# Kernel optimization log

Hardware: AMD Instinct MI355X
Metric: run time of the kernel (lower is better)

## Reference

```python
import jax, jax.numpy as jnp
import numpy as np

BS = 128  # block size for weight scale blocks

def dequant_block(w, s):
    # w: [O, I] fp8-valued weights (stored fp32 here); s: [O/BS, I/BS] per-block scale_inv
    O, I = w.shape
    sf = jnp.repeat(jnp.repeat(s, BS, axis=0), BS, axis=1)[:O, :I]
    return w * sf

def setup_inputs() -> dict:
    key = jax.random.key(0)
    ks = jax.random.split(key, 7)
    T, H, F = 512, 7168, 2048
    x = jax.random.normal(ks[0], (T, H), dtype=jnp.float32)
    w_gate = jax.random.normal(ks[1], (F, H), dtype=jnp.float32)
    s_gate = jax.random.uniform(ks[2], (F // BS, H // BS), dtype=jnp.float32, minval=0.01, maxval=0.05)
    w_up = jax.random.normal(ks[3], (F, H), dtype=jnp.float32)
    s_up = jax.random.uniform(ks[4], (F // BS, H // BS), dtype=jnp.float32, minval=0.01, maxval=0.05)
    w_down = jax.random.normal(ks[5], (H, F), dtype=jnp.float32)
    s_down = jax.random.uniform(ks[6], (H // BS, F // BS), dtype=jnp.float32, minval=0.01, maxval=0.05)
    return {"x": x, "w_gate": w_gate, "s_gate": s_gate, "w_up": w_up, "s_up": s_up,
            "w_down": w_down, "s_down": s_down}

def reference(x, w_gate, s_gate, w_up, s_up, w_down, s_down):
    # SwiGLU MLP with block-dequantized FP8 weights: down(silu(gate(x)) * up(x))
    wg = dequant_block(w_gate, s_gate)   # [F, H]
    wu = dequant_block(w_up, s_up)       # [F, H]
    wd = dequant_block(w_down, s_down)   # [H, F]
    g = x @ wg.T                          # [T, F]
    u = x @ wu.T                          # [T, F]
    h = jax.nn.silu(g) * u                # [T, F]
    return h @ wd.T                       # [T, H]
```

## Files before the change

### kernel.cpp

```cpp
#include <hip/hip_runtime.h>
#include <hip/hip_bf16.h>

typedef __bf16 bf16x8_t __attribute__((ext_vector_type(8)));
typedef float f32x4_t __attribute__((ext_vector_type(4)));

#define MFMA_BF16(a, b, c) __builtin_amdgcn_mfma_f32_16x16x32_bf16((a), (b), (c), 0, 0, 0)
#define VMW(N) asm volatile("s_waitcnt vmcnt(" #N ")" ::: "memory")
#define BARRIER() __builtin_amdgcn_s_barrier()

static constexpr int T_DIM = 512;
static constexpr int H_DIM = 7168;
static constexpr int F_DIM = 2048;

__device__ __forceinline__ ushort f2bf(float f) {
    return __builtin_bit_cast(ushort, __float2bfloat16(f));
}

__device__ __forceinline__ void gload_lds16(const void* g, void* l) {
    __builtin_amdgcn_global_load_lds(
        (const __attribute__((address_space(1))) unsigned int*)g,
        (__attribute__((address_space(3))) unsigned int*)(uintptr_t)l,
        16, 0, 0);
}

__global__ void cvt_x_kernel(const float* __restrict__ in, ushort* __restrict__ outp, int n4) {
    int i = blockIdx.x * 256 + threadIdx.x;
    if (i < n4) {
        float4 v = reinterpret_cast<const float4*>(in)[i];
        ushort4 o;
        o.x = f2bf(v.x); o.y = f2bf(v.y); o.z = f2bf(v.z); o.w = f2bf(v.w);
        reinterpret_cast<ushort4*>(outp)[i] = o;
    }
}

__global__ __launch_bounds__(512, 2) void gate_up_kernel(
    const ushort* __restrict__ xb, const float* __restrict__ wg,
    const float* __restrict__ sg, const float* __restrict__ wu,
    const float* __restrict__ su, float* __restrict__ gp, int NTS)
{
    __shared__ ushort As[2][256 * 64];
    __shared__ float  Bs[2][128 * 64];

    const int tid = threadIdx.x;
    const int lane = tid & 63;
    const int wid = tid >> 6;
    const int wr = wid >> 1, wc = wid & 1;
    const int bn = blockIdx.x, bm = blockIdx.y, bz = blockIdx.z;
    const int m0 = bm * 256;
    const int ks0 = bz * NTS, ks1 = ks0 + NTS;

    const float* __restrict__ Wb = (bn < 16) ? wg : wu;
    const float* __restrict__ srow = ((bn < 16) ? sg : su) + (size_t)(bn & 15) * (H_DIM / 128);
    const int nb = (bn & 15) * 128;

    f32x4_t acc[4][4] = {};

    const int a_r = tid >> 3, a_cu = tid & 7;
    const int b_r = tid >> 4, b_c32 = (tid & 15) >> 1, b_half = tid & 1;

    auto STAGE = [&](int kt, int bb) {
        const int k0 = kt * 64;
        #pragma unroll
        for (int q = 0; q < 4; ++q) {
            const int row = q * 64 + a_r;
            gload_lds16(&xb[(size_t)(m0 + row) * H_DIM + k0 + ((a_cu ^ (row & 7)) << 3)],
                        &As[bb][(q * 8192 + tid * 16) >> 1]);
        }
        #pragma unroll
        for (int q = 0; q < 4; ++q) {
            const int row = q * 32 + b_r;
            gload_lds16(&Wb[(size_t)(nb + row) * H_DIM + k0 + ((b_c32 ^ (row & 7)) << 3) + (b_half << 2)],
                        &Bs[bb][(q * 8192 + tid * 16) >> 2]);
        }
    };

    auto COMPUTE = [&](int bb) {
        #pragma unroll
        for (int ks = 0; ks < 2; ++ks) {
            const int kk = ks * 4 + (lane >> 4);
            bf16x8_t af[4];
            #pragma unroll
            for (int i = 0; i < 4; ++i) {
                const int row = wr * 64 + i * 16 + (lane & 15);
                af[i] = *reinterpret_cast<const bf16x8_t*>(&As[bb][row * 64 + ((kk ^ (row & 7)) << 3)]);
            }
            #pragma unroll
            for (int j = 0; j < 4; ++j) {
                const int row = wc * 64 + j * 16 + (lane & 15);
                const int u = kk ^ (row & 7);
                f32x4_t b0 = *reinterpret_cast<const f32x4_t*>(&Bs[bb][row * 64 + u * 8]);
                f32x4_t b1 = *reinterpret_cast<const f32x4_t*>(&Bs[bb][row * 64 + u * 8 + 4]);
                bf16x8_t bf;
                #pragma unroll
                for (int e = 0; e < 4; ++e) {
                    bf[e]     = (__bf16)b0[e];
                    bf[e + 4] = (__bf16)b1[e];
                }
                #pragma unroll
                for (int i = 0; i < 4; ++i)
                    acc[i][j] = MFMA_BF16(af[i], bf, acc[i][j]);
            }
        }
    };

    float s_cur = srow[ks0 >> 1];

    STAGE(ks0, 0);
    STAGE(ks0 + 1, 1);
    int bb = 0;
    for (int kt = ks0; kt < ks1; ++kt) {
        if (kt + 1 < ks1) { VMW(8); }
        else              { VMW(0); }
        BARRIER();
        if (((kt & 1) == 0) && kt > ks0) {
            const float s_new = srow[kt >> 1];
            const float r = s_cur / s_new;
            #pragma unroll
            for (int i = 0; i < 4; ++i)
                #pragma unroll
                for (int j = 0; j < 4; ++j)
                    acc[i][j] *= r;
            s_cur = s_new;
        }
        COMPUTE(bb);
        if (kt + 2 < ks1) {
            BARRIER();
            STAGE(kt + 2, bb);
        }
        bb ^= 1;
    }

    #pragma unroll
    for (int i = 0; i < 4; ++i)
        #pragma unroll
        for (int j = 0; j < 4; ++j)
            #pragma unroll
            for (int r = 0; r < 4; ++r) {
                const int m = m0 + wr * 64 + i * 16 + (lane >> 4) * 4 + r;
                const int nc = bn * 128 + wc * 64 + j * 16 + (lane & 15);
                gp[(size_t)bz * T_DIM * 4096 + (size_t)m * 4096 + nc] = acc[i][j][r] * s_cur;
            }
}

__global__ void h_reduce_kernel(const float* __restrict__ gp, ushort* __restrict__ hb,
                                int nsplit, int n4) {
    int i = blockIdx.x * 256 + threadIdx.x;
    if (i >= n4) return;
    const int m = i >> 9;
    const int c4 = i & 511;
    const size_t base = (size_t)m * 4096 + c4 * 4;
    const size_t stride = (size_t)T_DIM * 4096;
    float4 g = *reinterpret_cast<const float4*>(&gp[base]);
    float4 u = *reinterpret_cast<const float4*>(&gp[base + 2048]);
    for (int s = 1; s < nsplit; ++s) {
        float4 g2 = *reinterpret_cast<const float4*>(&gp[s * stride + base]);
        float4 u2 = *reinterpret_cast<const float4*>(&gp[s * stride + base + 2048]);
        g.x += g2.x; g.y += g2.y; g.z += g2.z; g.w += g2.w;
        u.x += u2.x; u.y += u2.y; u.z += u2.z; u.w += u2.w;
    }
    ushort4 o;
    o.x = f2bf(g.x / (1.0f + __expf(-g.x)) * u.x);
    o.y = f2bf(g.y / (1.0f + __expf(-g.y)) * u.y);
    o.z = f2bf(g.z / (1.0f + __expf(-g.z)) * u.z);
    o.w = f2bf(g.w / (1.0f + __expf(-g.w)) * u.w);
    reinterpret_cast<ushort4*>(hb)[i] = o;
}

template <bool DIRECT>
__global__ __launch_bounds__(512, 2) void down_kernel(
    const ushort* __restrict__ hb, const float* __restrict__ wd,
    const float* __restrict__ sd, float* __restrict__ outp, int NTS)
{
    __shared__ ushort As[2][128 * 64];
    __shared__ float  Bs[2][128 * 64];

    const int tid = threadIdx.x;
    const int lane = tid & 63;
    const int wid = tid >> 6;
    const int wr = wid >> 1, wc = wid & 1;
    const int bn = blockIdx.x, bm = blockIdx.y, bz = blockIdx.z;
    const int m0 = bm * 128;
    const float* __restrict__ srow = sd + (size_t)bn * (F_DIM / 128);
    const int nb = bn * 128;
    const int ks0 = bz * NTS, ks1 = ks0 + NTS;

    f32x4_t acc[2][4] = {};

    const int a_r = tid >> 3, a_cu = tid & 7;
    const int b_r = tid >> 4, b_c32 = (tid & 15) >> 1, b_half = tid & 1;

    auto STAGE = [&](int kt, int bb) {
        const int k0 = kt * 64;
        #pragma unroll
        for (int q = 0; q < 2; ++q) {
            const int row = q * 64 + a_r;
            gload_lds16(&hb[(size_t)(m0 + row) * F_DIM + k0 + ((a_cu ^ (row & 7)) << 3)],
                        &As[bb][(q * 8192 + tid * 16) >> 1]);
        }
        #pragma unroll
        for (int q = 0; q < 4; ++q) {
            const int row = q * 32 + b_r;
            gload_lds16(&wd[(size_t)(nb + row) * F_DIM + k0 + ((b_c32 ^ (row & 7)) << 3) + (b_half << 2)],
                        &Bs[bb][(q * 8192 + tid * 16) >> 2]);
        }
    };

    auto COMPUTE = [&](int bb) {
        #pragma unroll
        for (int ks = 0; ks < 2; ++ks) {
            const int kk = ks * 4 + (lane >> 4);
            bf16x8_t af[2];
            #pragma unroll
            for (int i = 0; i < 2; ++i) {
                const int row = wr * 32 + i * 16 + (lane & 15);
                af[i] = *reinterpret_cast<const bf16x8_t*>(&As[bb][row * 64 + ((kk ^ (row & 7)) << 3)]);
            }
            #pragma unroll
            for (int j = 0; j < 4; ++j) {
                const int row = wc * 64 + j * 16 + (lane & 15);
                const int u = kk ^ (row & 7);
                f32x4_t b0 = *reinterpret_cast<const f32x4_t*>(&Bs[bb][row * 64 + u * 8]);
                f32x4_t b1 = *reinterpret_cast<const f32x4_t*>(&Bs[bb][row * 64 + u * 8 + 4]);
                bf16x8_t bf;
                #pragma unroll
                for (int e = 0; e < 4; ++e) {
                    bf[e]     = (__bf16)b0[e];
                    bf[e + 4] = (__bf16)b1[e];
                }
                #pragma unroll
                for (int i = 0; i < 2; ++i)
                    acc[i][j] = MFMA_BF16(af[i], bf, acc[i][j]);
            }
        }
    };

    float s_cur = srow[ks0 >> 1];

    STAGE(ks0, 0);
    STAGE(ks0 + 1, 1);
    int bb = 0;
    for (int kt = ks0; kt < ks1; ++kt) {
        if (kt + 1 < ks1) { VMW(6); }
        else              { VMW(0); }
        BARRIER();
        if (((kt & 1) == 0) && kt > ks0) {
            const float s_new = srow[kt >> 1];
            const float r = s_cur / s_new;
            #pragma unroll
            for (int i = 0; i < 2; ++i)
                #pragma unroll
                for (int j = 0; j < 4; ++j)
                    acc[i][j] *= r;
            s_cur = s_new;
        }
        COMPUTE(bb);
        if (kt + 2 < ks1) {
            BARRIER();
            STAGE(kt + 2, bb);
        }
        bb ^= 1;
    }

    #pragma unroll
    for (int i = 0; i < 2; ++i)
        #pragma unroll
        for (int j = 0; j < 4; ++j)
            #pragma unroll
            for (int r = 0; r < 4; ++r) {
                const int m = m0 + wr * 32 + i * 16 + (lane >> 4) * 4 + r;
                const int nc = nb + wc * 64 + j * 16 + (lane & 15);
                const float v = acc[i][j][r] * s_cur;
                if (DIRECT)
                    outp[(size_t)m * H_DIM + nc] = v;
                else
                    outp[(size_t)bz * T_DIM * H_DIM + (size_t)m * H_DIM + nc] = v;
            }
}

__global__ void d_reduce_kernel(const float* __restrict__ dp, float* __restrict__ out, int n4) {
    int i = blockIdx.x * 256 + threadIdx.x;
    if (i >= n4) return;
    const size_t stride4 = (size_t)T_DIM * H_DIM / 4;
    float4 a = reinterpret_cast<const float4*>(dp)[i];
    float4 b = reinterpret_cast<const float4*>(dp)[i + stride4];
    a.x += b.x; a.y += b.y; a.z += b.z; a.w += b.w;
    reinterpret_cast<float4*>(out)[i] = a;
}

extern "C" void kernel_launch(void* const* d_in, const int* in_sizes, int n_in,
                              void* d_out, int out_size, void* d_ws, size_t ws_size,
                              hipStream_t stream) {
    const float* x  = (const float*)d_in[0];
    const float* wg = (const float*)d_in[1];
    const float* sg = (const float*)d_in[2];
    const float* wu = (const float*)d_in[3];
    const float* su = (const float*)d_in[4];
    const float* wd = (const float*)d_in[5];
    const float* sd = (const float*)d_in[6];
    float* out = (float*)d_out;

    ushort* xb = (ushort*)d_ws;
    ushort* hb = xb + (size_t)T_DIM * H_DIM;
    float*  gp = (float*)(hb + (size_t)T_DIM * F_DIM);

    const size_t base_b = (size_t)T_DIM * H_DIM * 2 + (size_t)T_DIM * F_DIM * 2;
    const size_t split_b = (size_t)T_DIM * 4096 * 4;

    int nsplit = 1;
    if (ws_size >= base_b + 4 * split_b) nsplit = 4;
    else if (ws_size >= base_b + 2 * split_b) nsplit = 2;

    const int n4x = T_DIM * H_DIM / 4;
    cvt_x_kernel<<<n4x / 256, 256, 0, stream>>>(x, xb, n4x);

    gate_up_kernel<<<dim3(32, T_DIM / 256, nsplit), 512, 0, stream>>>(
        xb, wg, sg, wu, su, gp, (H_DIM / 64) / nsplit);

    const int n4h = T_DIM * F_DIM / 4;
    h_reduce_kernel<<<n4h / 256, 256, 0, stream>>>(gp, hb, nsplit, n4h);

    const bool dsplit = (size_t)nsplit * split_b >= (size_t)2 * T_DIM * H_DIM * 4;
    if (dsplit) {
        float* dp = gp;
        down_kernel<false><<<dim3(H_DIM / 128, T_DIM / 128, 2), 512, 0, stream>>>(
            hb, wd, sd, dp, (F_DIM / 64) / 2);
        const int n4d = T_DIM * H_DIM / 4;
        d_reduce_kernel<<<n4d / 256, 256, 0, stream>>>(dp, out, n4d);
    } else {
        down_kernel<true><<<dim3(H_DIM / 128, T_DIM / 128, 1), 512, 0, stream>>>(
            hb, wd, sd, out, F_DIM / 64);
    }
}
```

Measured before the change: 110.1 us.

## Enlarge gate/up and down GEMM tiles to cut fp32 weight reloads

```diff
diff --git a/kernel.cpp b/kernel.cpp
--- a/kernel.cpp
+++ b/kernel.cpp
@@ -38,36 +38,40 @@
     const float* __restrict__ sg, const float* __restrict__ wu,
     const float* __restrict__ su, float* __restrict__ gp, int NTS)
 {
-    __shared__ ushort As[2][256 * 64];
-    __shared__ float  Bs[2][128 * 64];
+    __shared__ ushort As[256 * 64];
+    __shared__ float  Bs[2][256 * 64];
 
     const int tid = threadIdx.x;
     const int lane = tid & 63;
     const int wid = tid >> 6;
-    const int wr = wid >> 1, wc = wid & 1;
+    const int wr = wid >> 2, wcn = wid & 3;
     const int bn = blockIdx.x, bm = blockIdx.y, bz = blockIdx.z;
     const int m0 = bm * 256;
     const int ks0 = bz * NTS, ks1 = ks0 + NTS;
 
-    const float* __restrict__ Wb = (bn < 16) ? wg : wu;
-    const float* __restrict__ srow = ((bn < 16) ? sg : su) + (size_t)(bn & 15) * (H_DIM / 128);
-    const int nb = (bn & 15) * 128;
-
-    f32x4_t acc[4][4] = {};
+    const float* __restrict__ Wb = (bn < 8) ? wg : wu;
+    const float* __restrict__ srow = ((bn < 8) ? sg : su)
+        + (size_t)((bn & 7) * 2 + (wcn >> 1)) * (H_DIM / 128);
+    const int nb = (bn & 7) * 256;
+
+    f32x4_t acc[8][4] = {};
 
     const int a_r = tid >> 3, a_cu = tid & 7;
     const int b_r = tid >> 4, b_c32 = (tid & 15) >> 1, b_half = tid & 1;
 
-    auto STAGE = [&](int kt, int bb) {
+    auto STAGE_A = [&](int kt) {
         const int k0 = kt * 64;
         #pragma unroll
         for (int q = 0; q < 4; ++q) {
             const int row = q * 64 + a_r;
             gload_lds16(&xb[(size_t)(m0 + row) * H_DIM + k0 + ((a_cu ^ (row & 7)) << 3)],
-                        &As[bb][(q * 8192 + tid * 16) >> 1]);
-        }
-        #pragma unroll
-        for (int q = 0; q < 4; ++q) {
+                        &As[(q * 8192 + tid * 16) >> 1]);
+        }
+    };
+    auto STAGE_B = [&](int kt, int bb) {
+        const int k0 = kt * 64;
+        #pragma unroll
+        for (int q = 0; q < 8; ++q) {
             const int row = q * 32 + b_r;
             gload_lds16(&Wb[(size_t)(nb + row) * H_DIM + k0 + ((b_c32 ^ (row & 7)) << 3) + (b_half << 2)],
                         &Bs[bb][(q * 8192 + tid * 16) >> 2]);
@@ -78,15 +82,15 @@
         #pragma unroll
         for (int ks = 0; ks < 2; ++ks) {
             const int kk = ks * 4 + (lane >> 4);
-            bf16x8_t af[4];
-            #pragma unroll
-            for (int i = 0; i < 4; ++i) {
-                const int row = wr * 64 + i * 16 + (lane & 15);
-                af[i] = *reinterpret_cast<const bf16x8_t*>(&As[bb][row * 64 + ((kk ^ (row & 7)) << 3)]);
+            bf16x8_t af[8];
+            #pragma unroll
+            for (int i = 0; i < 8; ++i) {
+                const int row = wr * 128 + i * 16 + (lane & 15);
+                af[i] = *reinterpret_cast<const bf16x8_t*>(&As[row * 64 + ((kk ^ (row & 7)) << 3)]);
             }
             #pragma unroll
             for (int j = 0; j < 4; ++j) {
-                const int row = wc * 64 + j * 16 + (lane & 15);
+                const int row = wcn * 64 + j * 16 + (lane & 15);
                 const int u = kk ^ (row & 7);
                 f32x4_t b0 = *reinterpret_cast<const f32x4_t*>(&Bs[bb][row * 64 + u * 8]);
                 f32x4_t b1 = *reinterpret_cast<const f32x4_t*>(&Bs[bb][row * 64 + u * 8 + 4]);
@@ -97,7 +101,7 @@
                     bf[e + 4] = (__bf16)b1[e];
                 }
                 #pragma unroll
-                for (int i = 0; i < 4; ++i)
+                for (int i = 0; i < 8; ++i)
                     acc[i][j] = MFMA_BF16(af[i], bf, acc[i][j]);
             }
         }
@@ -105,39 +109,47 @@
 
     float s_cur = srow[ks0 >> 1];
 
-    STAGE(ks0, 0);
-    STAGE(ks0 + 1, 1);
+    STAGE_A(ks0);
+    STAGE_B(ks0, 0);
+    STAGE_B(ks0 + 1, 1);
+    VMW(8);
+    BARRIER();
+
     int bb = 0;
     for (int kt = ks0; kt < ks1; ++kt) {
-        if (kt + 1 < ks1) { VMW(8); }
-        else              { VMW(0); }
-        BARRIER();
         if (((kt & 1) == 0) && kt > ks0) {
             const float s_new = srow[kt >> 1];
             const float r = s_cur / s_new;
             #pragma unroll
-            for (int i = 0; i < 4; ++i)
+            for (int i = 0; i < 8; ++i)
                 #pragma unroll
                 for (int j = 0; j < 4; ++j)
                     acc[i][j] *= r;
             s_cur = s_new;
         }
         COMPUTE(bb);
-        if (kt + 2 < ks1) {
+        BARRIER();
+        if (kt + 1 < ks1) {
+            STAGE_A(kt + 1);
+            if (kt + 2 < ks1) {
+                STAGE_B(kt + 2, bb);
+                VMW(8);
+            } else {
+                VMW(0);
+            }
             BARRIER();
-            STAGE(kt + 2, bb);
         }
         bb ^= 1;
     }
 
     #pragma unroll
-    for (int i = 0; i < 4; ++i)
+    for (int i = 0; i < 8; ++i)
         #pragma unroll
         for (int j = 0; j < 4; ++j)
             #pragma unroll
             for (int r = 0; r < 4; ++r) {
-                const int m = m0 + wr * 64 + i * 16 + (lane >> 4) * 4 + r;
-                const int nc = bn * 128 + wc * 64 + j * 16 + (lane & 15);
+                const int m = m0 + wr * 128 + i * 16 + (lane >> 4) * 4 + r;
+                const int nc = bn * 256 + wcn * 64 + j * 16 + (lane & 15);
                 gp[(size_t)bz * T_DIM * 4096 + (size_t)m * 4096 + nc] = acc[i][j][r] * s_cur;
             }
 }
@@ -171,7 +183,7 @@
     const ushort* __restrict__ hb, const float* __restrict__ wd,
     const float* __restrict__ sd, float* __restrict__ outp, int NTS)
 {
-    __shared__ ushort As[2][128 * 64];
+    __shared__ ushort As[2][256 * 64];
     __shared__ float  Bs[2][128 * 64];
 
     const int tid = threadIdx.x;
@@ -179,12 +191,12 @@
     const int wid = tid >> 6;
     const int wr = wid >> 1, wc = wid & 1;
     const int bn = blockIdx.x, bm = blockIdx.y, bz = blockIdx.z;
-    const int m0 = bm * 128;
+    const int m0 = bm * 256;
     const float* __restrict__ srow = sd + (size_t)bn * (F_DIM / 128);
     const int nb = bn * 128;
     const int ks0 = bz * NTS, ks1 = ks0 + NTS;
 
-    f32x4_t acc[2][4] = {};
+    f32x4_t acc[4][4] = {};
 
     const int a_r = tid >> 3, a_cu = tid & 7;
     const int b_r = tid >> 4, b_c32 = (tid & 15) >> 1, b_half = tid & 1;
@@ -192,7 +204,7 @@
     auto STAGE = [&](int kt, int bb) {
         const int k0 = kt * 64;
         #pragma unroll
-        for (int q = 0; q < 2; ++q) {
+        for (int q = 0; q < 4; ++q) {
             const int row = q * 64 + a_r;
             gload_lds16(&hb[(size_t)(m0 + row) * F_DIM + k0 + ((a_cu ^ (row & 7)) << 3)],
                         &As[bb][(q * 8192 + tid * 16) >> 1]);
@@ -209,10 +221,10 @@
         #pragma unroll
         for (int ks = 0; ks < 2; ++ks) {
             const int kk = ks * 4 + (lane >> 4);
-            bf16x8_t af[2];
-            #pragma unroll
-            for (int i = 0; i < 2; ++i) {
-                const int row = wr * 32 + i * 16 + (lane & 15);
+            bf16x8_t af[4];
+            #pragma unroll
+            for (int i = 0; i < 4; ++i) {
+                const int row = wr * 64 + i * 16 + (lane & 15);
                 af[i] = *reinterpret_cast<const bf16x8_t*>(&As[bb][row * 64 + ((kk ^ (row & 7)) << 3)]);
             }
             #pragma unroll
@@ -228,7 +240,7 @@
                     bf[e + 4] = (__bf16)b1[e];
                 }
                 #pragma unroll
-                for (int i = 0; i < 2; ++i)
+                for (int i = 0; i < 4; ++i)
                     acc[i][j] = MFMA_BF16(af[i], bf, acc[i][j]);
             }
         }
@@ -240,14 +252,14 @@
     STAGE(ks0 + 1, 1);
     int bb = 0;
     for (int kt = ks0; kt < ks1; ++kt) {
-        if (kt + 1 < ks1) { VMW(6); }
+        if (kt + 1 < ks1) { VMW(8); }
         else              { VMW(0); }
         BARRIER();
         if (((kt & 1) == 0) && kt > ks0) {
             const float s_new = srow[kt >> 1];
             const float r = s_cur / s_new;
             #pragma unroll
-            for (int i = 0; i < 2; ++i)
+            for (int i = 0; i < 4; ++i)
                 #pragma unroll
                 for (int j = 0; j < 4; ++j)
                     acc[i][j] *= r;
@@ -262,12 +274,12 @@
     }
 
     #pragma unroll
-    for (int i = 0; i < 2; ++i)
+    for (int i = 0; i < 4; ++i)
         #pragma unroll
         for (int j = 0; j < 4; ++j)
             #pragma unroll
             for (int r = 0; r < 4; ++r) {
-                const int m = m0 + wr * 32 + i * 16 + (lane >> 4) * 4 + r;
+                const int m = m0 + wr * 64 + i * 16 + (lane >> 4) * 4 + r;
                 const int nc = nb + wc * 64 + j * 16 + (lane & 15);
                 const float v = acc[i][j][r] * s_cur;
                 if (DIRECT)
@@ -313,7 +325,7 @@
     const int n4x = T_DIM * H_DIM / 4;
     cvt_x_kernel<<<n4x / 256, 256, 0, stream>>>(x, xb, n4x);
 
-    gate_up_kernel<<<dim3(32, T_DIM / 256, nsplit), 512, 0, stream>>>(
+    gate_up_kernel<<<dim3(16, T_DIM / 256, nsplit), 512, 0, stream>>>(
         xb, wg, sg, wu, su, gp, (H_DIM / 64) / nsplit);
 
     const int n4h = T_DIM * F_DIM / 4;
@@ -322,12 +334,12 @@
     const bool dsplit = (size_t)nsplit * split_b >= (size_t)2 * T_DIM * H_DIM * 4;
     if (dsplit) {
         float* dp = gp;
-        down_kernel<false><<<dim3(H_DIM / 128, T_DIM / 128, 2), 512, 0, stream>>>(
+        down_kernel<false><<<dim3(H_DIM / 128, T_DIM / 256, 2), 512, 0, stream>>>(
             hb, wd, sd, dp, (F_DIM / 64) / 2);
         const int n4d = T_DIM * H_DIM / 4;
         d_reduce_kernel<<<n4d / 256, 256, 0, stream>>>(dp, out, n4d);
     } else {
-        down_kernel<true><<<dim3(H_DIM / 128, T_DIM / 128, 1), 512, 0, stream>>>(
+        down_kernel<true><<<dim3(H_DIM / 128, T_DIM / 256, 1), 512, 0, stream>>>(
             hb, wd, sd, out, F_DIM / 64);
     }
 }
```

Result: slower. 133.5 us (+21.3%).

## Stage fp32 weights through registers, convert to bf16 once into LDS

Applied to the files above, without the earlier changes.

```diff
diff --git a/kernel.cpp b/kernel.cpp
--- a/kernel.cpp
+++ b/kernel.cpp
@@ -6,6 +6,7 @@
 
 #define MFMA_BF16(a, b, c) __builtin_amdgcn_mfma_f32_16x16x32_bf16((a), (b), (c), 0, 0, 0)
 #define VMW(N) asm volatile("s_waitcnt vmcnt(" #N ")" ::: "memory")
+#define LGKM0() asm volatile("s_waitcnt lgkmcnt(0)" ::: "memory")
 #define BARRIER() __builtin_amdgcn_s_barrier()
 
 static constexpr int T_DIM = 512;
@@ -33,20 +34,20 @@
     }
 }
 
-__global__ __launch_bounds__(512, 2) void gate_up_kernel(
+__global__ __launch_bounds__(256, 2) void gate_up_kernel(
     const ushort* __restrict__ xb, const float* __restrict__ wg,
     const float* __restrict__ sg, const float* __restrict__ wu,
     const float* __restrict__ su, float* __restrict__ gp, int NTS)
 {
-    __shared__ ushort As[2][256 * 64];
-    __shared__ float  Bs[2][128 * 64];
+    __shared__ ushort As[2][128 * 64];
+    __shared__ ushort Bs[2][128 * 64];
 
     const int tid = threadIdx.x;
     const int lane = tid & 63;
     const int wid = tid >> 6;
     const int wr = wid >> 1, wc = wid & 1;
     const int bn = blockIdx.x, bm = blockIdx.y, bz = blockIdx.z;
-    const int m0 = bm * 256;
+    const int m0 = bm * 128;
     const int ks0 = bz * NTS, ks1 = ks0 + NTS;
 
     const float* __restrict__ Wb = (bn < 16) ? wg : wu;
@@ -56,21 +57,34 @@
     f32x4_t acc[4][4] = {};
 
     const int a_r = tid >> 3, a_cu = tid & 7;
-    const int b_r = tid >> 4, b_c32 = (tid & 15) >> 1, b_half = tid & 1;
-
-    auto STAGE = [&](int kt, int bb) {
+    const int b_row = tid >> 1, b_half = tid & 1;
+
+    auto ISSUE = [&](int kt, f32x4_t (&rb)[8], int buf) {
         const int k0 = kt * 64;
+        const float* src = &Wb[(size_t)(nb + b_row) * H_DIM + k0 + b_half * 32];
+        #pragma unroll
+        for (int q = 0; q < 8; ++q)
+            rb[q] = reinterpret_cast<const f32x4_t*>(src)[q];
         #pragma unroll
         for (int q = 0; q < 4; ++q) {
-            const int row = q * 64 + a_r;
+            const int row = q * 32 + a_r;
             gload_lds16(&xb[(size_t)(m0 + row) * H_DIM + k0 + ((a_cu ^ (row & 7)) << 3)],
-                        &As[bb][(q * 8192 + tid * 16) >> 1]);
-        }
+                        &As[buf][q * 2048 + tid * 8]);
+        }
+    };
+
+    auto CVTW = [&](f32x4_t (&rb)[8], int buf) {
         #pragma unroll
         for (int q = 0; q < 4; ++q) {
-            const int row = q * 32 + b_r;
-            gload_lds16(&Wb[(size_t)(nb + row) * H_DIM + k0 + ((b_c32 ^ (row & 7)) << 3) + (b_half << 2)],
-                        &Bs[bb][(q * 8192 + tid * 16) >> 2]);
+            bf16x8_t v;
+            #pragma unroll
+            for (int e = 0; e < 4; ++e) {
+                v[e]     = (__bf16)rb[2 * q][e];
+                v[e + 4] = (__bf16)rb[2 * q + 1][e];
+            }
+            const int c16 = b_half * 4 + q;
+            *reinterpret_cast<bf16x8_t*>(
+                &Bs[buf][b_row * 64 + ((c16 ^ (b_row & 7)) << 3)]) = v;
         }
     };
 
@@ -78,7 +92,7 @@
         #pragma unroll
         for (int ks = 0; ks < 2; ++ks) {
             const int kk = ks * 4 + (lane >> 4);
-            bf16x8_t af[4];
+            bf16x8_t af[4], bf[4];
             #pragma unroll
             for (int i = 0; i < 4; ++i) {
                 const int row = wr * 64 + i * 16 + (lane & 15);
@@ -87,47 +101,56 @@
             #pragma unroll
             for (int j = 0; j < 4; ++j) {
                 const int row = wc * 64 + j * 16 + (lane & 15);
-                const int u = kk ^ (row & 7);
-                f32x4_t b0 = *reinterpret_cast<const f32x4_t*>(&Bs[bb][row * 64 + u * 8]);
-                f32x4_t b1 = *reinterpret_cast<const f32x4_t*>(&Bs[bb][row * 64 + u * 8 + 4]);
-                bf16x8_t bf;
-                #pragma unroll
-                for (int e = 0; e < 4; ++e) {
-                    bf[e]     = (__bf16)b0[e];
-                    bf[e + 4] = (__bf16)b1[e];
-                }
-                #pragma unroll
-                for (int i = 0; i < 4; ++i)
-                    acc[i][j] = MFMA_BF16(af[i], bf, acc[i][j]);
-            }
-        }
-    };
-
-    float s_cur = srow[ks0 >> 1];
-
-    STAGE(ks0, 0);
-    STAGE(ks0 + 1, 1);
-    int bb = 0;
-    for (int kt = ks0; kt < ks1; ++kt) {
-        if (kt + 1 < ks1) { VMW(8); }
-        else              { VMW(0); }
-        BARRIER();
-        if (((kt & 1) == 0) && kt > ks0) {
-            const float s_new = srow[kt >> 1];
-            const float r = s_cur / s_new;
+                bf[j] = *reinterpret_cast<const bf16x8_t*>(&Bs[bb][row * 64 + ((kk ^ (row & 7)) << 3)]);
+            }
             #pragma unroll
             for (int i = 0; i < 4; ++i)
                 #pragma unroll
                 for (int j = 0; j < 4; ++j)
-                    acc[i][j] *= r;
-            s_cur = s_new;
-        }
-        COMPUTE(bb);
-        if (kt + 2 < ks1) {
-            BARRIER();
-            STAGE(kt + 2, bb);
-        }
-        bb ^= 1;
+                    acc[i][j] = MFMA_BF16(af[i], bf[j], acc[i][j]);
+        }
+    };
+
+    float s_cur = srow[ks0 >> 1];
+    auto RESCALE = [&](int kt) {
+        const float s_new = srow[kt >> 1];
+        const float r = s_cur / s_new;
+        #pragma unroll
+        for (int i = 0; i < 4; ++i)
+            #pragma unroll
+            for (int j = 0; j < 4; ++j)
+                acc[i][j] *= r;
+        s_cur = s_new;
+    };
+
+    f32x4_t rb0[8], rb1[8];
+
+    ISSUE(ks0, rb0, 0);
+    ISSUE(ks0 + 1, rb1, 1);
+    VMW(16);
+    CVTW(rb0, 0);
+    VMW(12);
+    LGKM0();
+    BARRIER();
+
+    for (int kt = ks0; kt < ks1; kt += 2) {
+        if (kt > ks0) RESCALE(kt);
+        VMW(4);
+        CVTW(rb1, 1);
+        COMPUTE(0);
+        LGKM0();
+        BARRIER();
+        if (kt + 2 < ks1) { ISSUE(kt + 2, rb0, 0); VMW(12); }
+        else              { VMW(0); }
+        BARRIER();
+
+        if (kt + 2 < ks1) { VMW(4); CVTW(rb0, 0); }
+        COMPUTE(1);
+        LGKM0();
+        BARRIER();
+        if (kt + 3 < ks1) { ISSUE(kt + 3, rb1, 1); VMW(12); }
+        else              { VMW(0); }
+        BARRIER();
     }
 
     #pragma unroll
@@ -167,12 +190,12 @@
 }
 
 template <bool DIRECT>
-__global__ __launch_bounds__(512, 2) void down_kernel(
+__global__ __launch_bounds__(256, 2) void down_kernel(
     const ushort* __restrict__ hb, const float* __restrict__ wd,
     const float* __restrict__ sd, float* __restrict__ outp, int NTS)
 {
     __shared__ ushort As[2][128 * 64];
-    __shared__ float  Bs[2][128 * 64];
+    __shared__ ushort Bs[2][128 * 64];
 
     const int tid = threadIdx.x;
     const int lane = tid & 63;
@@ -184,24 +207,37 @@
     const int nb = bn * 128;
     const int ks0 = bz * NTS, ks1 = ks0 + NTS;
 
-    f32x4_t acc[2][4] = {};
+    f32x4_t acc[4][4] = {};
 
     const int a_r = tid >> 3, a_cu = tid & 7;
-    const int b_r = tid >> 4, b_c32 = (tid & 15) >> 1, b_half = tid & 1;
-
-    auto STAGE = [&](int kt, int bb) {
+    const int b_row = tid >> 1, b_half = tid & 1;
+
+    auto ISSUE = [&](int kt, f32x4_t (&rb)[8], int buf) {
         const int k0 = kt * 64;
-        #pragma unroll
-        for (int q = 0; q < 2; ++q) {
-            const int row = q * 64 + a_r;
+        const float* src = &wd[(size_t)(nb + b_row) * F_DIM + k0 + b_half * 32];
+        #pragma unroll
+        for (int q = 0; q < 8; ++q)
+            rb[q] = reinterpret_cast<const f32x4_t*>(src)[q];
+        #pragma unroll
+        for (int q = 0; q < 4; ++q) {
+            const int row = q * 32 + a_r;
             gload_lds16(&hb[(size_t)(m0 + row) * F_DIM + k0 + ((a_cu ^ (row & 7)) << 3)],
-                        &As[bb][(q * 8192 + tid * 16) >> 1]);
-        }
+                        &As[buf][q * 2048 + tid * 8]);
+        }
+    };
+
+    auto CVTW = [&](f32x4_t (&rb)[8], int buf) {
         #pragma unroll
         for (int q = 0; q < 4; ++q) {
-            const int row = q * 32 + b_r;
-            gload_lds16(&wd[(size_t)(nb + row) * F_DIM + k0 + ((b_c32 ^ (row & 7)) << 3) + (b_half << 2)],
-                        &Bs[bb][(q * 8192 + tid * 16) >> 2]);
+            bf16x8_t v;
+            #pragma unroll
+            for (int e = 0; e < 4; ++e) {
+                v[e]     = (__bf16)rb[2 * q][e];
+                v[e + 4] = (__bf16)rb[2 * q + 1][e];
+            }
+            const int c16 = b_half * 4 + q;
+            *reinterpret_cast<bf16x8_t*>(
+                &Bs[buf][b_row * 64 + ((c16 ^ (b_row & 7)) << 3)]) = v;
         }
     };
 
@@ -209,65 +245,74 @@
         #pragma unroll
         for (int ks = 0; ks < 2; ++ks) {
             const int kk = ks * 4 + (lane >> 4);
-            bf16x8_t af[2];
-            #pragma unroll
-            for (int i = 0; i < 2; ++i) {
-                const int row = wr * 32 + i * 16 + (lane & 15);
+            bf16x8_t af[4], bf[4];
+            #pragma unroll
+            for (int i = 0; i < 4; ++i) {
+                const int row = wr * 64 + i * 16 + (lane & 15);
                 af[i] = *reinterpret_cast<const bf16x8_t*>(&As[bb][row * 64 + ((kk ^ (row & 7)) << 3)]);
             }
             #pragma unroll
             for (int j = 0; j < 4; ++j) {
                 const int row = wc * 64 + j * 16 + (lane & 15);
-                const int u = kk ^ (row & 7);
-                f32x4_t b0 = *reinterpret_cast<const f32x4_t*>(&Bs[bb][row * 64 + u * 8]);
-                f32x4_t b1 = *reinterpret_cast<const f32x4_t*>(&Bs[bb][row * 64 + u * 8 + 4]);
-                bf16x8_t bf;
-                #pragma unroll
-                for (int e = 0; e < 4; ++e) {
-                    bf[e]     = (__bf16)b0[e];
-                    bf[e + 4] = (__bf16)b1[e];
-                }
-                #pragma unroll
-                for (int i = 0; i < 2; ++i)
-                    acc[i][j] = MFMA_BF16(af[i], bf, acc[i][j]);
-            }
-        }
-    };
-
-    float s_cur = srow[ks0 >> 1];
-
-    STAGE(ks0, 0);
-    STAGE(ks0 + 1, 1);
-    int bb = 0;
-    for (int kt = ks0; kt < ks1; ++kt) {
-        if (kt + 1 < ks1) { VMW(6); }
-        else              { VMW(0); }
-        BARRIER();
-        if (((kt & 1) == 0) && kt > ks0) {
-            const float s_new = srow[kt >> 1];
-            const float r = s_cur / s_new;
-            #pragma unroll
-            for (int i = 0; i < 2; ++i)
+                bf[j] = *reinterpret_cast<const bf16x8_t*>(&Bs[bb][row * 64 + ((kk ^ (row & 7)) << 3)]);
+            }
+            #pragma unroll
+            for (int i = 0; i < 4; ++i)
                 #pragma unroll
                 for (int j = 0; j < 4; ++j)
-                    acc[i][j] *= r;
-            s_cur = s_new;
-        }
-        COMPUTE(bb);
-        if (kt + 2 < ks1) {
-            BARRIER();
-            STAGE(kt + 2, bb);
-        }
-        bb ^= 1;
+                    acc[i][j] = MFMA_BF16(af[i], bf[j], acc[i][j]);
+        }
+    };
+
+    float s_cur = srow[ks0 >> 1];
+    auto RESCALE = [&](int kt) {
+        const float s_new = srow[kt >> 1];
+        const float r = s_cur / s_new;
+        #pragma unroll
+        for (int i = 0; i < 4; ++i)
+            #pragma unroll
+            for (int j = 0; j < 4; ++j)
+                acc[i][j] *= r;
+        s_cur = s_new;
+    };
+
+    f32x4_t rb0[8], rb1[8];
+
+    ISSUE(ks0, rb0, 0);
+    ISSUE(ks0 + 1, rb1, 1);
+    VMW(16);
+    CVTW(rb0, 0);
+    VMW(12);
+    LGKM0();
+    BARRIER();
+
+    for (int kt = ks0; kt < ks1; kt += 2) {
+        if (kt > ks0) RESCALE(kt);
+        VMW(4);
+        CVTW(rb1, 1);
+        COMPUTE(0);
+        LGKM0();
+        BARRIER();
+        if (kt + 2 < ks1) { ISSUE(kt + 2, rb0, 0); VMW(12); }
+        else              { VMW(0); }
+        BARRIER();
+
+        if (kt + 2 < ks1) { VMW(4); CVTW(rb0, 0); }
+        COMPUTE(1);
+        LGKM0();
+        BARRIER();
+        if (kt + 3 < ks1) { ISSUE(kt + 3, rb1, 1); VMW(12); }
+        else              { VMW(0); }
+        BARRIER();
     }
 
     #pragma unroll
-    for (int i = 0; i < 2; ++i)
+    for (int i = 0; i < 4; ++i)
         #pragma unroll
         for (int j = 0; j < 4; ++j)
             #pragma unroll
             for (int r = 0; r < 4; ++r) {
-                const int m = m0 + wr * 32 + i * 16 + (lane >> 4) * 4 + r;
+                const int m = m0 + wr * 64 + i * 16 + (lane >> 4) * 4 + r;
                 const int nc = nb + wc * 64 + j * 16 + (lane & 15);
                 const float v = acc[i][j][r] * s_cur;
                 if (DIRECT)
@@ -313,7 +358,7 @@
     const int n4x = T_DIM * H_DIM / 4;
     cvt_x_kernel<<<n4x / 256, 256, 0, stream>>>(x, xb, n4x);
 
-    gate_up_kernel<<<dim3(32, T_DIM / 256, nsplit), 512, 0, stream>>>(
+    gate_up_kernel<<<dim3(32, T_DIM / 128, nsplit), 256, 0, stream>>>(
         xb, wg, sg, wu, su, gp, (H_DIM / 64) / nsplit);
 
     const int n4h = T_DIM * F_DIM / 4;
@@ -322,12 +367,12 @@
     const bool dsplit = (size_t)nsplit * split_b >= (size_t)2 * T_DIM * H_DIM * 4;
     if (dsplit) {
         float* dp = gp;
-        down_kernel<false><<<dim3(H_DIM / 128, T_DIM / 128, 2), 512, 0, stream>>>(
+        down_kernel<false><<<dim3(H_DIM / 128, T_DIM / 128, 2), 256, 0, stream>>>(
             hb, wd, sd, dp, (F_DIM / 64) / 2);
         const int n4d = T_DIM * H_DIM / 4;
         d_reduce_kernel<<<n4d / 256, 256, 0, stream>>>(dp, out, n4d);
     } else {
-        down_kernel<true><<<dim3(H_DIM / 128, T_DIM / 128, 1), 512, 0, stream>>>(
+        down_kernel<true><<<dim3(H_DIM / 128, T_DIM / 128, 1), 256, 0, stream>>>(
             hb, wd, sd, out, F_DIM / 64);
     }
 }
```

Result: slower. 164.0 us (+49.0%).
